# Optimization experiments

Hardware: AMD Instinct MI355X
Metric: run time of the kernel (lower is better)

Reference implementation:

```python
import jax, jax.numpy as jnp
import numpy as np

B, C, H, W = 2, 32, 128, 128
K = 5            # window_size
NH = 2           # num_heads
HD = C // NH     # head_dim = 16
KK = K * K
HID = int(2 * C * 2.0)  # mlp hidden = dim*2*mlp_ratio = 128
SCALE = HD ** -0.5


def _ln(x, w, b, eps=1e-5):
    m = jnp.mean(x, -1, keepdims=True)
    v = jnp.var(x, -1, keepdims=True)
    return (x - m) * jax.lax.rsqrt(v + eps) * w + b


def _windows(t):
    # t: [B,H,W,C] -> [B,H,W,C,K*K]; zero-padded KxK neighborhood per pixel
    # (same layout as nn.Unfold: kernel position is the fastest-varying axis).
    p = (K - 1) // 2
    Hc, Wc = t.shape[1], t.shape[2]
    tp = jnp.pad(t, ((0, 0), (p, p), (p, p), (0, 0)))
    return jnp.stack([tp[:, i:i + Hc, j:j + Wc, :] for i in range(K) for j in range(K)], axis=-1)


def _rel_index():
    # Swin-style relative position index for a KxK window -> [KK,KK] ints
    c = jnp.stack(jnp.meshgrid(jnp.arange(K), jnp.arange(K), indexing='ij'), 0).reshape(2, -1)
    r = (c[:, :, None] - c[:, None, :]).transpose(1, 2, 0) + (K - 1)
    return r[..., 0] * (2 * K - 1) + r[..., 1]


def _ckbd_mask(h, w):
    # checkerboard attention mask: [L, KK, KK] additive (0 or -100)
    ck = jnp.zeros((h, w), jnp.float32)
    ck = ck.at[0::2, 1::2].set(1.0).at[1::2, 0::2].set(1.0)
    cw = _windows(ck[None, :, :, None])[0, :, :, 0, :].reshape(h * w, KK)  # [L,KK]
    m = cw[:, :, None] * cw[:, None, :]
    return jnp.where(m == 1.0, 0.0, -100.0)


def setup_inputs() -> dict:
    key = jax.random.key(0)
    ks = jax.random.split(key, 8)
    p = lambda k, s: (0.02 * jax.random.normal(k, s)).astype(jnp.float32)
    return dict(
        x=jax.random.normal(ks[0], (B, C, H, W), dtype=jnp.float32),
        qkv_w=p(ks[1], (3 * C, C)), qkv_b=jnp.zeros((3 * C,), jnp.float32),
        rel_table=p(ks[2], ((2 * K - 1) ** 2, NH)),
        norm1_w=jnp.ones((C,), jnp.float32), norm1_b=jnp.zeros((C,), jnp.float32),
        norm2_w=jnp.ones((2 * C,), jnp.float32), norm2_b=jnp.zeros((2 * C,), jnp.float32),
        proj_w=p(ks[3], (2 * C, 2 * C)), proj_b=jnp.zeros((2 * C,), jnp.float32),
        fusion_w=p(ks[4], (2 * C, C, K, K)), fusion_b=jnp.zeros((2 * C,), jnp.float32),
        mlp_w1=p(ks[5], (HID, 2 * C)), mlp_b1=jnp.zeros((HID,), jnp.float32),
        mlp_w2=p(ks[6], (2 * C, HID)), mlp_b2=jnp.zeros((2 * C,), jnp.float32),
    )


def reference(x, qkv_w, qkv_b, rel_table, norm1_w, norm1_b, norm2_w, norm2_b,
              proj_w, proj_b, fusion_w, fusion_b, mlp_w1, mlp_b1, mlp_w2, mlp_b2):
    Bs, Cs, Hs, Ws = x.shape
    L = Hs * Ws
    xt = x.reshape(Bs, Cs, L).transpose(0, 2, 1)          # [B,L,C]
    xn = _ln(xt, norm1_w, norm1_b)
    qkv = jnp.einsum('blc,oc->blo', xn, qkv_w) + qkv_b     # [B,L,3C]
    qkv = qkv.reshape(Bs, Hs, Ws, 3, Cs)
    q, k, v = qkv[..., 0, :], qkv[..., 1, :], qkv[..., 2, :]  # each [B,H,W,C]

    def heads(t):
        # windows -> [B,L,C,KK]; split C as (head_dim, num_heads) to match the
        # original reshape(B,L,head_dim,num_heads,KK).permute(0,1,3,4,2)
        w_ = _windows(t).reshape(Bs, L, HD, NH, KK)
        return w_.transpose(0, 1, 3, 4, 2)                 # [B,L,nh,KK,hd]

    qh, kh, vh = heads(q), heads(k), heads(v)
    attn = jnp.einsum('blhqd,blhkd->blhqk', qh * SCALE, kh)  # [B,L,nh,KK,KK]

    bias = rel_table[_rel_index().reshape(-1)].reshape(KK, KK, NH).transpose(2, 0, 1)
    attn = attn + bias[None, None]
    attn = attn + _ckbd_mask(Hs, Ws)[None, :, None]
    attn = jax.nn.softmax(attn, axis=-1)

    o = jnp.einsum('blhqk,blhkd->blhqd', attn, vh)           # [B,L,nh,KK,hd]
    # -> [B,L,K,K,nh,hd] -> [B,L,K,K,C] (head-major channel order, as in torch)
    o = o.reshape(Bs, L, NH, K, K, HD).transpose(0, 1, 3, 4, 2, 5).reshape(Bs, L, K, K, Cs)
    # fusion: Conv2d(C, 2C, kernel=K) on [BL,C,K,K] with no padding == full contraction
    y = jnp.einsum('blijc,ocij->blo', o, fusion_w) + fusion_b  # [B,L,2C]
    y = jnp.einsum('blc,oc->blo', y, proj_w) + proj_b
    h1 = _ln(y, norm2_w, norm2_b)
    mlp = jnp.einsum('blh,oh->blo',
                     jax.nn.gelu(jnp.einsum('blc,hc->blh', h1, mlp_w1) + mlp_b1, approximate=False),
                     mlp_w2) + mlp_b2
    y = y + mlp
    return y.transpose(0, 2, 1).reshape(Bs, 2 * Cs, Hs, Ws)
```

## Files before the change

kernel.cpp:

```cpp
#include <hip/hip_runtime.h>
#include <cstdint>
#include <cstddef>

#define HH 128
#define WW 128
#define LL 16384
#define BL 32768

typedef float  f32x4  __attribute__((ext_vector_type(4)));
typedef __fp16 h2     __attribute__((ext_vector_type(2)));
typedef __fp16 h8     __attribute__((ext_vector_type(8)));

union U32H { unsigned u; h2 h; };

static __device__ __forceinline__ float fdot2(h2 a, h2 b, float c) {
  return __builtin_amdgcn_fdot2(a, b, c, false);
}
static __device__ __forceinline__ unsigned pkh2(float a, float b) {
  h2 h = __builtin_amdgcn_cvt_pkrtz(a, b);
  U32H t; t.h = h; return t.u;
}
static __device__ __forceinline__ h2 bcasth(float a) {
  return __builtin_amdgcn_cvt_pkrtz(a, a);
}
static __device__ __forceinline__ unsigned short f2h(float x) {
  union { __fp16 h; unsigned short u; } c; c.h = (__fp16)x; return c.u;
}

#define LOADH8(dst, ptr) { \
  uint4 _a = *(const uint4*)(ptr); uint4 _b = *(const uint4*)((ptr)+8); U32H _t; \
  _t.u=_a.x; dst[0]=_t.h; _t.u=_a.y; dst[1]=_t.h; _t.u=_a.z; dst[2]=_t.h; _t.u=_a.w; dst[3]=_t.h; \
  _t.u=_b.x; dst[4]=_t.h; _t.u=_b.y; dst[5]=_t.h; _t.u=_b.z; dst[6]=_t.h; _t.u=_b.w; dst[7]=_t.h; }

__global__ __launch_bounds__(256) void k_combine(
    const float* __restrict__ proj_w, const float* __restrict__ proj_b,
    const float* __restrict__ fw, const float* __restrict__ fb,
    const float* __restrict__ w1, const float* __restrict__ w2,
    unsigned short* __restrict__ wctT, float* __restrict__ bc,
    unsigned short* __restrict__ w1h, unsigned short* __restrict__ w2h)
{
  if (blockIdx.x == 200) {
    int o = threadIdx.x;
    if (o < 64) {
      float acc = proj_b[o];
      for (int m = 0; m < 64; ++m) acc = fmaf(proj_w[o*64+m], fb[m], acc);
      bc[o] = acc;
    }
    return;
  }
  if (blockIdx.x == 201) {
    for (int i = threadIdx.x; i < 8192; i += 256) w1h[i] = f2h(w1[i]);
    return;
  }
  if (blockIdx.x == 202) {
    for (int i = threadIdx.x; i < 8192; i += 256) w2h[i] = f2h(w2[i]);
    return;
  }
  int gid = blockIdx.x * 256 + threadIdx.x;
  int o  = gid / 800;
  int kk = gid - o * 800;
  int c  = kk & 31;
  int t  = kk >> 5;
  int in = c * 25 + t;
  float acc = 0.f;
  for (int m = 0; m < 64; ++m) acc = fmaf(proj_w[o*64+m], fw[m*800+in], acc);
  wctT[gid] = f2h(acc);
}

__global__ __launch_bounds__(128) void k_ln_qkv(
    const float* __restrict__ x, const float* __restrict__ qkv_w,
    const float* __restrict__ qkv_b, const float* __restrict__ n1w,
    const float* __restrict__ n1b, unsigned short* __restrict__ qo,
    unsigned short* __restrict__ ko, unsigned short* __restrict__ vo)
{
  __shared__ float sW[32*32];
  __shared__ float sB[32];
  __shared__ float sNw[32], sNb[32];
  int p = blockIdx.y;
  for (int i = threadIdx.x; i < 32*32; i += 128) sW[i] = qkv_w[p*1024 + i];
  if (threadIdx.x < 32) {
    sB[threadIdx.x]  = qkv_b[p*32 + threadIdx.x];
    sNw[threadIdx.x] = n1w[threadIdx.x];
    sNb[threadIdx.x] = n1b[threadIdx.x];
  }
  __syncthreads();
  int gid = blockIdx.x * 128 + threadIdx.x;
  int b = gid >> 14, l = gid & (LL - 1);
  const float* xp = x + (size_t)b * 32 * LL + l;
  float xv[32];
  float mean = 0.f;
  #pragma unroll
  for (int c = 0; c < 32; ++c) { xv[c] = xp[(size_t)c * LL]; mean += xv[c]; }
  mean *= 0.03125f;
  float var = 0.f;
  #pragma unroll
  for (int c = 0; c < 32; ++c) { float d = xv[c] - mean; var = fmaf(d, d, var); }
  float rs = rsqrtf(var * 0.03125f + 1e-5f);
  #pragma unroll
  for (int c = 0; c < 32; ++c) xv[c] = (xv[c] - mean) * rs * sNw[c] + sNb[c];
  float ao[32];
  #pragma unroll
  for (int o = 0; o < 32; ++o) {
    const float* wr = &sW[o * 32];
    float acc = sB[o];
    #pragma unroll
    for (int c = 0; c < 32; ++c) acc = fmaf(xv[c], wr[c], acc);
    ao[(o & 1) * 16 + (o >> 1)] = acc;
  }
  unsigned short* op = (p == 0 ? qo : p == 1 ? ko : vo) + (size_t)gid * 32;
  #pragma unroll
  for (int e = 0; e < 4; ++e) {
    uint4 pk4;
    pk4.x = pkh2(ao[e*8+0], ao[e*8+1]);
    pk4.y = pkh2(ao[e*8+2], ao[e*8+3]);
    pk4.z = pkh2(ao[e*8+4], ao[e*8+5]);
    pk4.w = pkh2(ao[e*8+6], ao[e*8+7]);
    *(uint4*)(op + e*8) = pk4;
  }
}

#define TH 4
#define TW 8
#define NPOS 96
#define KVSTR 24
#define OSTRU 524

template<int MODE>
static __device__ __forceinline__ void attn_pair(
    int tqA, int tqB, int nh, bool wA, bool wB,
    int posb, int sOrow, int klbase,
    const unsigned short* __restrict__ sQ, const unsigned short* __restrict__ sK,
    const unsigned short* __restrict__ sV, unsigned short* __restrict__ sO,
    const float* __restrict__ sRT, const float* __restrict__ sPar)
{
  const int nhb = nh * 96;
  int iqA = tqA / 5, jqA = tqA - iqA * 5;
  int iqB = tqB / 5, jqB = tqB - iqB * 5;
  int pqA = posb + iqA * 12 + jqA;
  int pqB = posb + iqB * 12 + jqB;
  float parqA = 0.f, parqB = 0.f;
  if (MODE == 3) { parqA = sPar[pqA]; parqB = sPar[pqB]; }
  h2 qA[8], qB[8];
  LOADH8(qA, &sQ[(nhb + pqA) * KVSTR]);
  LOADH8(qB, &sQ[(nhb + pqB) * KVSTR]);
  const int bbA = (iqA * 9 + jqA) * 2 + 80 + nh;
  const int bbB = (iqB * 9 + jqB) * 2 + 80 + nh;
  float sA = 0.f, sB = 0.f;
  h2 ooA[8], ooB[8];
  #pragma unroll
  for (int e = 0; e < 8; ++e) { ooA[e] = (h2)(__fp16)0.f; ooB[e] = (h2)(__fp16)0.f; }
  #pragma unroll 1
  for (int ik = 0; ik < 5; ++ik) {
    int pkrow = posb + ik * 12;
    int bA = bbA - ik * 18, bB = bbB - ik * 18;
    auto body = [&](int jk) {
      int pk = pkrow + jk;
      h2 kh[8];
      LOADH8(kh, &sK[(nhb + pk) * KVSTR]);
      float aA = 0.f, aB = 0.f;
      #pragma unroll
      for (int u = 0; u < 8; ++u) { aA = fdot2(qA[u], kh[u], aA); aB = fdot2(qB[u], kh[u], aB); }
      float biasA = sRT[bA - 2 * jk], biasB = sRT[bB - 2 * jk];
      float eA, eB;
      if (MODE == 3) {
        float park = sPar[pk];
        float mk = (park == 1.f) ? 0.f : -100.f;
        eA = __expf(fmaf(parqA, mk, fmaf(aA, 0.25f, biasA)));
        eB = __expf(fmaf(parqB, mk, fmaf(aB, 0.25f, biasB)));
      } else {
        eA = __expf(fmaf(aA, 0.25f, biasA));
        eB = __expf(fmaf(aB, 0.25f, biasB));
      }
      sA += eA; sB += eB;
      h2 eAh = bcasth(eA), eBh = bcasth(eB);
      h2 vh[8];
      LOADH8(vh, &sV[(nhb + pk) * KVSTR]);
      #pragma unroll
      for (int u = 0; u < 8; ++u) { ooA[u] = eAh * vh[u] + ooA[u]; ooB[u] = eBh * vh[u] + ooB[u]; }
    };
    if (MODE == 0 || MODE == 3) {
      body(0); body(1); body(2); body(3); body(4);
    } else if (MODE == 1) {
      if ((ik & 1) == 0) { body(1); body(3); }
      else { body(0); body(2); body(4); }
    } else {
      if ((ik & 1) == 0) { body(0); body(2); body(4); }
      else { body(1); body(3); }
    }
  }
  if (wA) {
    h2 ih = bcasth(1.f / sA);
    int kl = (tqA - klbase) * 32 + nh * 16;
    union { h2 h[8]; uint4 u4[2]; } R;
    #pragma unroll
    for (int u = 0; u < 8; ++u) R.h[u] = ooA[u] * ih;
    *(uint4*)&sO[sOrow * OSTRU + kl] = R.u4[0];
    *(uint4*)&sO[sOrow * OSTRU + kl + 8] = R.u4[1];
  }
  if (wB) {
    h2 ih = bcasth(1.f / sB);
    int kl = (tqB - klbase) * 32 + nh * 16;
    union { h2 h[8]; uint4 u4[2]; } R;
    #pragma unroll
    for (int u = 0; u < 8; ++u) R.h[u] = ooB[u] * ih;
    *(uint4*)&sO[sOrow * OSTRU + kl] = R.u4[0];
    *(uint4*)&sO[sOrow * OSTRU + kl + 8] = R.u4[1];
  }
}

__global__ __launch_bounds__(256, 3) void k_attn(
    const unsigned short* __restrict__ qi, const unsigned short* __restrict__ ki,
    const unsigned short* __restrict__ vi, const float* __restrict__ rel_table,
    const unsigned short* __restrict__ wctT, const float* __restrict__ bc,
    float* __restrict__ y2)
{
  __shared__ __align__(16) unsigned short sQ[192*KVSTR];
  __shared__ __align__(16) unsigned short sK[192*KVSTR];
  __shared__ __align__(16) unsigned short sV[192*KVSTR];
  __shared__ __align__(16) unsigned short sO[32*OSTRU];
  __shared__ float sRT[162];
  __shared__ float sPar[NPOS];

  int tid = threadIdx.x;
  int lane = tid & 63, wv = tid >> 6;
  int b  = blockIdx.z;
  int h0 = blockIdx.y * TH, w0 = blockIdx.x * TW;
  bool fastb = (blockIdx.y >= 1) && (blockIdx.y <= 30) && (blockIdx.x >= 1) && (blockIdx.x <= 14);

  for (int i = tid; i < 162; i += 256) sRT[i] = rel_table[i];
  if (tid < NPOS) {
    int ph = tid / 12, pw = tid - ph * 12;
    int h2v = h0 + ph - 2, w2v = w0 + pw - 2;
    bool valid = ((unsigned)h2v < HH) && ((unsigned)w2v < WW);
    sPar[tid] = (valid && (((h2v + w2v) & 1) == 1)) ? 1.f : 0.f;
  }
  for (int idx = tid; idx < 1152; idx += 256) {
    int arr = idx / 384;
    int rem = idx - arr * 384;
    int pos = rem >> 2, q4 = rem & 3;
    int nh = q4 >> 1, half = q4 & 1;
    int ph = pos / 12, pw = pos - ph * 12;
    int h2v = h0 + ph - 2, w2v = w0 + pw - 2;
    uint4 val = make_uint4(0u, 0u, 0u, 0u);
    if (((unsigned)h2v < HH) && ((unsigned)w2v < WW)) {
      const unsigned short* src = (arr == 0 ? ki : arr == 1 ? vi : qi)
                       + ((size_t)((b << 14) + (h2v << 7) + w2v)) * 32 + nh * 16 + half * 8;
      val = *(const uint4*)src;
    }
    unsigned short* dp = (arr == 0 ? sK : arr == 1 ? sV : sQ)
                       + (nh * 96 + pos) * KVSTR + half * 8;
    *(uint4*)dp = val;
  }
  __syncthreads();

  f32x4 acc[2] = {{0.f,0.f,0.f,0.f},{0.f,0.f,0.f,0.f}};
  int ocol = wv * 16 + (lane & 15);

  int cls = wv & 1;
  int l16 = lane & 15;
  int nh  = wv >> 1;
  int kk4 = lane >> 4;
  int ly  = l16 >> 2;
  int lx  = 2 * (l16 & 3) + ((cls + ly) & 1);
  int posb  = ly * 12 + lx;
  int sOrow = cls * 16 + l16;

  if (fastb) {
    if (cls == 0) {
      attn_pair<0>(4*kk4,   4*kk4+2, nh, true, true, posb, sOrow, 0, sQ, sK, sV, sO, sRT, sPar);
      attn_pair<1>(4*kk4+1, 4*kk4+3, nh, true, true, posb, sOrow, 0, sQ, sK, sV, sO, sRT, sPar);
    } else {
      attn_pair<0>(4*kk4+1, 4*kk4+3, nh, true, true, posb, sOrow, 0, sQ, sK, sV, sO, sRT, sPar);
      attn_pair<2>(4*kk4,   4*kk4+2, nh, true, true, posb, sOrow, 0, sQ, sK, sV, sO, sRT, sPar);
    }
  } else {
    attn_pair<3>(4*kk4,   4*kk4+2, nh, true, true, posb, sOrow, 0, sQ, sK, sV, sO, sRT, sPar);
    attn_pair<3>(4*kk4+1, 4*kk4+3, nh, true, true, posb, sOrow, 0, sQ, sK, sV, sO, sRT, sPar);
  }
  __syncthreads();
  {
    const unsigned short* bcol = wctT + (size_t)ocol * 800 + (lane >> 4) * 8;
    for (int kt = 0; kt < 16; ++kt) {
      h8 bfrag = *(const h8*)(bcol + kt * 32);
      #pragma unroll
      for (int mt = 0; mt < 2; ++mt) {
        h8 afrag = *(const h8*)&sO[(mt*16 + (lane & 15))*OSTRU + kt*32 + (lane >> 4)*8];
        acc[mt] = __builtin_amdgcn_mfma_f32_16x16x32_f16(afrag, bfrag, acc[mt], 0, 0, 0);
      }
    }
  }
  __syncthreads();

  {
    int LqA = 16, LqB = 18; bool LwA = false, LwB = false;
    int SqA = 17, SqB = 19; bool SwA = false, SwB = false;
    if (cls == 0) {
      if (kk4 == 0)      { LwA = LwB = true; SwA = SwB = true; }
      else if (kk4 == 1) { LqA = 20; LqB = 22; LwA = LwB = true; SqA = 21; SqB = 23; SwA = SwB = true; }
      else if (kk4 == 2) { LqA = 24; LqB = 24; LwA = true; }
    } else {
      if (kk4 == 0)      { LqA = 17; LqB = 19; LwA = LwB = true; SqA = 16; SqB = 18; SwA = SwB = true; }
      else if (kk4 == 1) { LqA = 21; LqB = 23; LwA = LwB = true; SqA = 20; SqB = 22; SwA = SwB = true; }
      else if (kk4 == 2) { SqA = 24; SqB = 24; SwA = true; }
    }
    if (fastb) {
      if (cls == 0) {
        attn_pair<0>(LqA, LqB, nh, LwA, LwB, posb, sOrow, 16, sQ, sK, sV, sO, sRT, sPar);
        attn_pair<1>(SqA, SqB, nh, SwA, SwB, posb, sOrow, 16, sQ, sK, sV, sO, sRT, sPar);
      } else {
        attn_pair<0>(LqA, LqB, nh, LwA, LwB, posb, sOrow, 16, sQ, sK, sV, sO, sRT, sPar);
        attn_pair<2>(SqA, SqB, nh, SwA, SwB, posb, sOrow, 16, sQ, sK, sV, sO, sRT, sPar);
      }
    } else {
      attn_pair<3>(LqA, LqB, nh, LwA, LwB, posb, sOrow, 16, sQ, sK, sV, sO, sRT, sPar);
      attn_pair<3>(SqA, SqB, nh, SwA, SwB, posb, sOrow, 16, sQ, sK, sV, sO, sRT, sPar);
    }
  }
  __syncthreads();
  {
    const unsigned short* bcol = wctT + (size_t)ocol * 800 + 512 + (lane >> 4) * 8;
    for (int kt = 0; kt < 9; ++kt) {
      h8 bfrag = *(const h8*)(bcol + kt * 32);
      #pragma unroll
      for (int mt = 0; mt < 2; ++mt) {
        h8 afrag = *(const h8*)&sO[(mt*16 + (lane & 15))*OSTRU + kt*32 + (lane >> 4)*8];
        acc[mt] = __builtin_amdgcn_mfma_f32_16x16x32_f16(afrag, bfrag, acc[mt], 0, 0, 0);
      }
    }
  }
  __syncthreads();

  float bco = bc[ocol];
  #pragma unroll
  for (int mt = 0; mt < 2; ++mt) {
    #pragma unroll
    for (int r2 = 0; r2 < 4; ++r2) {
      int ly2 = lane >> 4;
      int lx2 = 2 * r2 + ((mt + ly2) & 1);
      int gid = (b << 14) + ((h0 + ly2) << 7) + (w0 + lx2);
      y2[(size_t)gid * 64 + ocol] = acc[mt][r2] + bco;
    }
  }
}

__global__ __launch_bounds__(256) void k_mlp(
    const float* __restrict__ y2, const float* __restrict__ n2w,
    const float* __restrict__ n2b, const unsigned short* __restrict__ w1h,
    const float* __restrict__ b1, const unsigned short* __restrict__ w2h,
    const float* __restrict__ b2, float* __restrict__ out)
{
  __shared__ __align__(16) unsigned short sA[64*72];
  __shared__ __align__(16) unsigned short sH[64*136];
  int tid = threadIdx.x;
  int lane = tid & 63, wv = tid >> 6;
  int m0 = blockIdx.x * 64;
  {
    int r = tid >> 2, qd = tid & 3;
    const float* yp = y2 + (size_t)(m0 + r) * 64 + qd * 16;
    float xv[16];
    float s = 0.f;
    #pragma unroll
    for (int e = 0; e < 4; ++e) {
      float4 t4 = *(const float4*)(yp + e*4);
      xv[4*e] = t4.x; xv[4*e+1] = t4.y; xv[4*e+2] = t4.z; xv[4*e+3] = t4.w;
      s += t4.x + t4.y + t4.z + t4.w;
    }
    s += __shfl_xor(s, 1);
    s += __shfl_xor(s, 2);
    float mean = s * (1.f/64.f);
    float v = 0.f;
    #pragma unroll
    for (int e = 0; e < 16; ++e) { float d = xv[e] - mean; v = fmaf(d, d, v); }
    v += __shfl_xor(v, 1);
    v += __shfl_xor(v, 2);
    float rs = rsqrtf(v * (1.f/64.f) + 1e-5f);
    #pragma unroll
    for (int u = 0; u < 8; ++u) {
      int c0 = qd*16 + 2*u;
      float h0v = (xv[2*u]   - mean) * rs * n2w[c0]   + n2b[c0];
      float h1v = (xv[2*u+1] - mean) * rs * n2w[c0+1] + n2b[c0+1];
      *(unsigned*)&sA[r*72 + c0] = pkh2(h0v, h1v);
    }
  }
  __syncthreads();
  f32x4 acc1[4][2];
  #pragma unroll
  for (int mt = 0; mt < 4; ++mt)
    #pragma unroll
    for (int nt = 0; nt < 2; ++nt) acc1[mt][nt] = (f32x4){0.f,0.f,0.f,0.f};
  #pragma unroll
  for (int kt = 0; kt < 2; ++kt) {
    #pragma unroll
    for (int nt = 0; nt < 2; ++nt) {
      int ncol = wv*32 + nt*16 + (lane & 15);
      h8 bfrag = *(const h8*)(w1h + ncol*64 + kt*32 + (lane >> 4)*8);
      #pragma unroll
      for (int mt = 0; mt < 4; ++mt) {
        h8 afrag = *(const h8*)&sA[(mt*16 + (lane & 15))*72 + kt*32 + (lane >> 4)*8];
        acc1[mt][nt] = __builtin_amdgcn_mfma_f32_16x16x32_f16(afrag, bfrag, acc1[mt][nt], 0, 0, 0);
      }
    }
  }
  #pragma unroll
  for (int nt = 0; nt < 2; ++nt) {
    int ncol = wv*32 + nt*16 + (lane & 15);
    float b1v = b1[ncol];
    #pragma unroll
    for (int mt = 0; mt < 4; ++mt) {
      #pragma unroll
      for (int r2 = 0; r2 < 4; ++r2) {
        int mrow = mt*16 + (lane >> 4)*4 + r2;
        float h = acc1[mt][nt][r2] + b1v;
        float g = 0.5f * h * (1.f + erff(h * 0.70710678118f));
        sH[mrow*136 + ncol] = f2h(g);
      }
    }
  }
  __syncthreads();
  f32x4 acc2[4];
  #pragma unroll
  for (int mt = 0; mt < 4; ++mt) acc2[mt] = (f32x4){0.f,0.f,0.f,0.f};
  int ocol = wv*16 + (lane & 15);
  #pragma unroll
  for (int kt = 0; kt < 4; ++kt) {
    h8 bfrag = *(const h8*)(w2h + ocol*128 + kt*32 + (lane >> 4)*8);
    #pragma unroll
    for (int mt = 0; mt < 4; ++mt) {
      h8 afrag = *(const h8*)&sH[(mt*16 + (lane & 15))*136 + kt*32 + (lane >> 4)*8];
      acc2[mt] = __builtin_amdgcn_mfma_f32_16x16x32_f16(afrag, bfrag, acc2[mt], 0, 0, 0);
    }
  }
  float b2v = b2[ocol];
  int bb = m0 >> 14;
  #pragma unroll
  for (int mt = 0; mt < 4; ++mt) {
    int mrow = mt*16 + (lane >> 4)*4;
    int l = m0 + mrow;
    const float* yp = y2 + (size_t)l * 64 + ocol;
    float4 o4;
    o4.x = yp[0]   + acc2[mt][0] + b2v;
    o4.y = yp[64]  + acc2[mt][1] + b2v;
    o4.z = yp[128] + acc2[mt][2] + b2v;
    o4.w = yp[192] + acc2[mt][3] + b2v;
    *(float4*)&out[(size_t)bb * 64 * LL + (size_t)ocol * LL + (l - (bb << 14))] = o4;
  }
}

extern "C" void kernel_launch(void* const* d_in, const int* in_sizes, int n_in,
                              void* d_out, int out_size, void* d_ws, size_t ws_size,
                              hipStream_t stream) {
  const float* x         = (const float*)d_in[0];
  const float* qkv_w     = (const float*)d_in[1];
  const float* qkv_b     = (const float*)d_in[2];
  const float* rel_table = (const float*)d_in[3];
  const float* n1w       = (const float*)d_in[4];
  const float* n1b       = (const float*)d_in[5];
  const float* n2w       = (const float*)d_in[6];
  const float* n2b       = (const float*)d_in[7];
  const float* proj_w    = (const float*)d_in[8];
  const float* proj_b    = (const float*)d_in[9];
  const float* fw        = (const float*)d_in[10];
  const float* fb        = (const float*)d_in[11];
  const float* w1        = (const float*)d_in[12];
  const float* b1        = (const float*)d_in[13];
  const float* w2        = (const float*)d_in[14];
  const float* b2        = (const float*)d_in[15];

  char* ws = (char*)d_ws;
  unsigned short* q    = (unsigned short*)(ws);
  unsigned short* k    = (unsigned short*)(ws + 2097152);
  unsigned short* v    = (unsigned short*)(ws + 4194304);
  float*          y2   = (float*)(ws + 6291456);
  unsigned short* wctT = (unsigned short*)(ws + 14680064);
  float*          bc   = (float*)(ws + 14782464);
  unsigned short* w1h  = (unsigned short*)(ws + 14782720);
  unsigned short* w2h  = (unsigned short*)(ws + 14799104);
  float* out = (float*)d_out;

  k_combine<<<203, 256, 0, stream>>>(proj_w, proj_b, fw, fb, w1, w2, wctT, bc, w1h, w2h);
  k_ln_qkv<<<dim3(BL/128, 3), 128, 0, stream>>>(x, qkv_w, qkv_b, n1w, n1b, q, k, v);
  k_attn<<<dim3(WW/TW, HH/TH, 2), 256, 0, stream>>>(q, k, v, rel_table, wctT, bc, y2);
  k_mlp<<<BL/64, 256, 0, stream>>>(y2, n2w, n2b, w1h, b1, w2h, b2, out);
}
```

Before: 92.80 us.

## Halve attention tile height, read Q from global, restructure thread mapping

Shrinks the attention block tile from 4x8 to 2x8 pixels, which doubles the grid and cuts shared memory. Q is no longer staged in LDS and is read directly from global memory. The pair of queries per thread is reorganised into a long/short pair that shares K/V loads under the checkerboard parity, and launch bounds are raised to allow more resident blocks. The MLP kernel's row tile is also halved to 32 rows. Smaller tiles mean more halo reloads of K/V, and the uncoalesced per-thread global Q loads may cost latency.

```diff
diff --git a/kernel.cpp b/kernel.cpp
--- a/kernel.cpp
+++ b/kernel.cpp
@@ -119,105 +119,126 @@
   }
 }
 
-#define TH 4
+#define TH 2
 #define TW 8
-#define NPOS 96
+#define NPOS 72
 #define KVSTR 24
 #define OSTRU 524
 
-template<int MODE>
-static __device__ __forceinline__ void attn_pair(
-    int tqA, int tqB, int nh, bool wA, bool wB,
+template<int CLS, bool SLOW>
+static __device__ __forceinline__ void attn_ls(
+    int tqL, int tqS, bool wL, bool wS, int nh,
+    int h0, int w0, int ly, int lx, int b,
+    const unsigned short* __restrict__ qi,
     int posb, int sOrow, int klbase,
-    const unsigned short* __restrict__ sQ, const unsigned short* __restrict__ sK,
+    const unsigned short* __restrict__ sK,
     const unsigned short* __restrict__ sV, unsigned short* __restrict__ sO,
     const float* __restrict__ sRT, const float* __restrict__ sPar)
 {
-  const int nhb = nh * 96;
-  int iqA = tqA / 5, jqA = tqA - iqA * 5;
-  int iqB = tqB / 5, jqB = tqB - iqB * 5;
-  int pqA = posb + iqA * 12 + jqA;
-  int pqB = posb + iqB * 12 + jqB;
-  float parqA = 0.f, parqB = 0.f;
-  if (MODE == 3) { parqA = sPar[pqA]; parqB = sPar[pqB]; }
-  h2 qA[8], qB[8];
-  LOADH8(qA, &sQ[(nhb + pqA) * KVSTR]);
-  LOADH8(qB, &sQ[(nhb + pqB) * KVSTR]);
-  const int bbA = (iqA * 9 + jqA) * 2 + 80 + nh;
-  const int bbB = (iqB * 9 + jqB) * 2 + 80 + nh;
-  float sA = 0.f, sB = 0.f;
-  h2 ooA[8], ooB[8];
-  #pragma unroll
-  for (int e = 0; e < 8; ++e) { ooA[e] = (h2)(__fp16)0.f; ooB[e] = (h2)(__fp16)0.f; }
+  const int nhb = nh * 72;
+  int iqL = tqL / 5, jqL = tqL - iqL * 5;
+  int iqS = tqS / 5, jqS = tqS - iqS * 5;
+  int hqL = h0 + ly + iqL - 2, wqL = w0 + lx + jqL - 2;
+  int hqS = h0 + ly + iqS - 2, wqS = w0 + lx + jqS - 2;
+  h2 qL[8], qS[8];
+  float parqL = 0.f, parqS = 0.f;
+  if (SLOW) {
+    bool vL = ((unsigned)hqL < HH) && ((unsigned)wqL < WW);
+    bool vS = ((unsigned)hqS < HH) && ((unsigned)wqS < WW);
+    parqL = (vL && (((hqL + wqL) & 1) == 1)) ? 1.f : 0.f;
+    parqS = (vS && (((hqS + wqS) & 1) == 1)) ? 1.f : 0.f;
+    if (vL) {
+      LOADH8(qL, qi + ((size_t)((b<<14)+(hqL<<7)+wqL))*32 + nh*16);
+    } else {
+      for (int u = 0; u < 8; ++u) qL[u] = (h2)(__fp16)0.f;
+    }
+    if (vS) {
+      LOADH8(qS, qi + ((size_t)((b<<14)+(hqS<<7)+wqS))*32 + nh*16);
+    } else {
+      for (int u = 0; u < 8; ++u) qS[u] = (h2)(__fp16)0.f;
+    }
+  } else {
+    LOADH8(qL, qi + ((size_t)((b<<14)+(hqL<<7)+wqL))*32 + nh*16);
+    LOADH8(qS, qi + ((size_t)((b<<14)+(hqS<<7)+wqS))*32 + nh*16);
+  }
+  const int bbL = (iqL * 9 + jqL) * 2 + 80 + nh;
+  const int bbS = (iqS * 9 + jqS) * 2 + 80 + nh;
+  float sumL = 0.f, sumS = 0.f;
+  h2 ooL[8], ooS[8];
+  #pragma unroll
+  for (int e = 0; e < 8; ++e) { ooL[e] = (h2)(__fp16)0.f; ooS[e] = (h2)(__fp16)0.f; }
   #pragma unroll 1
   for (int ik = 0; ik < 5; ++ik) {
     int pkrow = posb + ik * 12;
-    int bA = bbA - ik * 18, bB = bbB - ik * 18;
-    auto body = [&](int jk) {
+    int bL = bbL - ik * 18, bS = bbS - ik * 18;
+    auto body = [&](int jk, bool doS) {
       int pk = pkrow + jk;
-      h2 kh[8];
-      LOADH8(kh, &sK[(nhb + pk) * KVSTR]);
-      float aA = 0.f, aB = 0.f;
-      #pragma unroll
-      for (int u = 0; u < 8; ++u) { aA = fdot2(qA[u], kh[u], aA); aB = fdot2(qB[u], kh[u], aB); }
-      float biasA = sRT[bA - 2 * jk], biasB = sRT[bB - 2 * jk];
-      float eA, eB;
-      if (MODE == 3) {
-        float park = sPar[pk];
-        float mk = (park == 1.f) ? 0.f : -100.f;
-        eA = __expf(fmaf(parqA, mk, fmaf(aA, 0.25f, biasA)));
-        eB = __expf(fmaf(parqB, mk, fmaf(aB, 0.25f, biasB)));
-      } else {
-        eA = __expf(fmaf(aA, 0.25f, biasA));
-        eB = __expf(fmaf(aB, 0.25f, biasB));
+      h2 kh[8]; LOADH8(kh, &sK[(nhb + pk) * KVSTR]);
+      h2 vh[8]; LOADH8(vh, &sV[(nhb + pk) * KVSTR]);
+      float mk = 0.f;
+      if (SLOW) { float park = sPar[pk]; mk = (park == 1.f) ? 0.f : -100.f; }
+      {
+        float a = 0.f;
+        #pragma unroll
+        for (int u = 0; u < 8; ++u) a = fdot2(qL[u], kh[u], a);
+        float e = SLOW ? __expf(fmaf(parqL, mk, fmaf(a, 0.25f, sRT[bL - 2*jk])))
+                       : __expf(fmaf(a, 0.25f, sRT[bL - 2*jk]));
+        sumL += e;
+        h2 eh = bcasth(e);
+        #pragma unroll
+        for (int u = 0; u < 8; ++u) ooL[u] = eh * vh[u] + ooL[u];
       }
-      sA += eA; sB += eB;
-      h2 eAh = bcasth(eA), eBh = bcasth(eB);
-      h2 vh[8];
-      LOADH8(vh, &sV[(nhb + pk) * KVSTR]);
-      #pragma unroll
-      for (int u = 0; u < 8; ++u) { ooA[u] = eAh * vh[u] + ooA[u]; ooB[u] = eBh * vh[u] + ooB[u]; }
+      if (doS) {
+        float a = 0.f;
+        #pragma unroll
+        for (int u = 0; u < 8; ++u) a = fdot2(qS[u], kh[u], a);
+        float e = SLOW ? __expf(fmaf(parqS, mk, fmaf(a, 0.25f, sRT[bS - 2*jk])))
+                       : __expf(fmaf(a, 0.25f, sRT[bS - 2*jk]));
+        sumS += e;
+        h2 eh = bcasth(e);
+        #pragma unroll
+        for (int u = 0; u < 8; ++u) ooS[u] = eh * vh[u] + ooS[u];
+      }
     };
-    if (MODE == 0 || MODE == 3) {
-      body(0); body(1); body(2); body(3); body(4);
-    } else if (MODE == 1) {
-      if ((ik & 1) == 0) { body(1); body(3); }
-      else { body(0); body(2); body(4); }
+    if (SLOW) {
+      body(0,true); body(1,true); body(2,true); body(3,true); body(4,true);
+    } else if (CLS == 0) {
+      if ((ik & 1) == 0) { body(0,false); body(1,true);  body(2,false); body(3,true);  body(4,false); }
+      else               { body(0,true);  body(1,false); body(2,true);  body(3,false); body(4,true); }
     } else {
-      if ((ik & 1) == 0) { body(0); body(2); body(4); }
-      else { body(1); body(3); }
-    }
-  }
-  if (wA) {
-    h2 ih = bcasth(1.f / sA);
-    int kl = (tqA - klbase) * 32 + nh * 16;
+      if ((ik & 1) == 0) { body(0,true);  body(1,false); body(2,true);  body(3,false); body(4,true); }
+      else               { body(0,false); body(1,true);  body(2,false); body(3,true);  body(4,false); }
+    }
+  }
+  if (wL) {
+    h2 ih = bcasth(1.f / sumL);
+    int kl = (tqL - klbase) * 32 + nh * 16;
     union { h2 h[8]; uint4 u4[2]; } R;
     #pragma unroll
-    for (int u = 0; u < 8; ++u) R.h[u] = ooA[u] * ih;
+    for (int u = 0; u < 8; ++u) R.h[u] = ooL[u] * ih;
     *(uint4*)&sO[sOrow * OSTRU + kl] = R.u4[0];
     *(uint4*)&sO[sOrow * OSTRU + kl + 8] = R.u4[1];
   }
-  if (wB) {
-    h2 ih = bcasth(1.f / sB);
-    int kl = (tqB - klbase) * 32 + nh * 16;
+  if (wS) {
+    h2 ih = bcasth(1.f / sumS);
+    int kl = (tqS - klbase) * 32 + nh * 16;
     union { h2 h[8]; uint4 u4[2]; } R;
     #pragma unroll
-    for (int u = 0; u < 8; ++u) R.h[u] = ooB[u] * ih;
+    for (int u = 0; u < 8; ++u) R.h[u] = ooS[u] * ih;
     *(uint4*)&sO[sOrow * OSTRU + kl] = R.u4[0];
     *(uint4*)&sO[sOrow * OSTRU + kl + 8] = R.u4[1];
   }
 }
 
-__global__ __launch_bounds__(256, 3) void k_attn(
+__global__ __launch_bounds__(256, 5) void k_attn(
     const unsigned short* __restrict__ qi, const unsigned short* __restrict__ ki,
     const unsigned short* __restrict__ vi, const float* __restrict__ rel_table,
     const unsigned short* __restrict__ wctT, const float* __restrict__ bc,
     float* __restrict__ y2)
 {
-  __shared__ __align__(16) unsigned short sQ[192*KVSTR];
-  __shared__ __align__(16) unsigned short sK[192*KVSTR];
-  __shared__ __align__(16) unsigned short sV[192*KVSTR];
-  __shared__ __align__(16) unsigned short sO[32*OSTRU];
+  __shared__ __align__(16) unsigned short sK[144*KVSTR];
+  __shared__ __align__(16) unsigned short sV[144*KVSTR];
+  __shared__ __align__(16) unsigned short sO[16*OSTRU];
   __shared__ float sRT[162];
   __shared__ float sPar[NPOS];
 
@@ -225,7 +246,7 @@
   int lane = tid & 63, wv = tid >> 6;
   int b  = blockIdx.z;
   int h0 = blockIdx.y * TH, w0 = blockIdx.x * TW;
-  bool fastb = (blockIdx.y >= 1) && (blockIdx.y <= 30) && (blockIdx.x >= 1) && (blockIdx.x <= 14);
+  bool fastb = (blockIdx.y >= 1) && (blockIdx.y <= 62) && (blockIdx.x >= 1) && (blockIdx.x <= 14);
 
   for (int i = tid; i < 162; i += 256) sRT[i] = rel_table[i];
   if (tid < NPOS) {
@@ -234,86 +255,69 @@
     bool valid = ((unsigned)h2v < HH) && ((unsigned)w2v < WW);
     sPar[tid] = (valid && (((h2v + w2v) & 1) == 1)) ? 1.f : 0.f;
   }
-  for (int idx = tid; idx < 1152; idx += 256) {
-    int arr = idx / 384;
-    int rem = idx - arr * 384;
+  for (int idx = tid; idx < 576; idx += 256) {
+    int arr = idx / 288;
+    int rem = idx - arr * 288;
     int pos = rem >> 2, q4 = rem & 3;
     int nh = q4 >> 1, half = q4 & 1;
     int ph = pos / 12, pw = pos - ph * 12;
     int h2v = h0 + ph - 2, w2v = w0 + pw - 2;
     uint4 val = make_uint4(0u, 0u, 0u, 0u);
     if (((unsigned)h2v < HH) && ((unsigned)w2v < WW)) {
-      const unsigned short* src = (arr == 0 ? ki : arr == 1 ? vi : qi)
+      const unsigned short* src = (arr == 0 ? ki : vi)
                        + ((size_t)((b << 14) + (h2v << 7) + w2v)) * 32 + nh * 16 + half * 8;
       val = *(const uint4*)src;
     }
-    unsigned short* dp = (arr == 0 ? sK : arr == 1 ? sV : sQ)
-                       + (nh * 96 + pos) * KVSTR + half * 8;
+    unsigned short* dp = (arr == 0 ? sK : sV) + (nh * 72 + pos) * KVSTR + half * 8;
     *(uint4*)dp = val;
   }
   __syncthreads();
 
-  f32x4 acc[2] = {{0.f,0.f,0.f,0.f},{0.f,0.f,0.f,0.f}};
+  f32x4 acc = {0.f, 0.f, 0.f, 0.f};
   int ocol = wv * 16 + (lane & 15);
 
   int cls = wv & 1;
-  int l16 = lane & 15;
   int nh  = wv >> 1;
-  int kk4 = lane >> 4;
-  int ly  = l16 >> 2;
-  int lx  = 2 * (l16 & 3) + ((cls + ly) & 1);
+  int l8  = lane & 7;
+  int r8  = lane >> 3;
+  int ly  = l8 >> 2;
+  int lx  = 2 * (l8 & 3) + ((cls + ly) & 1);
   int posb  = ly * 12 + lx;
-  int sOrow = cls * 16 + l16;
+  int sOrow = cls * 8 + l8;
 
   if (fastb) {
-    if (cls == 0) {
-      attn_pair<0>(4*kk4,   4*kk4+2, nh, true, true, posb, sOrow, 0, sQ, sK, sV, sO, sRT, sPar);
-      attn_pair<1>(4*kk4+1, 4*kk4+3, nh, true, true, posb, sOrow, 0, sQ, sK, sV, sO, sRT, sPar);
-    } else {
-      attn_pair<0>(4*kk4+1, 4*kk4+3, nh, true, true, posb, sOrow, 0, sQ, sK, sV, sO, sRT, sPar);
-      attn_pair<2>(4*kk4,   4*kk4+2, nh, true, true, posb, sOrow, 0, sQ, sK, sV, sO, sRT, sPar);
-    }
+    if (cls == 0) attn_ls<0,false>(2*r8,   2*r8+1, true, true, nh, h0,w0,ly,lx,b,qi, posb, sOrow, 0, sK, sV, sO, sRT, sPar);
+    else          attn_ls<1,false>(2*r8+1, 2*r8,   true, true, nh, h0,w0,ly,lx,b,qi, posb, sOrow, 0, sK, sV, sO, sRT, sPar);
   } else {
-    attn_pair<3>(4*kk4,   4*kk4+2, nh, true, true, posb, sOrow, 0, sQ, sK, sV, sO, sRT, sPar);
-    attn_pair<3>(4*kk4+1, 4*kk4+3, nh, true, true, posb, sOrow, 0, sQ, sK, sV, sO, sRT, sPar);
+    int tl = (cls == 0) ? 2*r8 : 2*r8+1;
+    int ts = (cls == 0) ? 2*r8+1 : 2*r8;
+    attn_ls<0,true>(tl, ts, true, true, nh, h0,w0,ly,lx,b,qi, posb, sOrow, 0, sK, sV, sO, sRT, sPar);
   }
   __syncthreads();
   {
     const unsigned short* bcol = wctT + (size_t)ocol * 800 + (lane >> 4) * 8;
     for (int kt = 0; kt < 16; ++kt) {
       h8 bfrag = *(const h8*)(bcol + kt * 32);
-      #pragma unroll
-      for (int mt = 0; mt < 2; ++mt) {
-        h8 afrag = *(const h8*)&sO[(mt*16 + (lane & 15))*OSTRU + kt*32 + (lane >> 4)*8];
-        acc[mt] = __builtin_amdgcn_mfma_f32_16x16x32_f16(afrag, bfrag, acc[mt], 0, 0, 0);
-      }
+      h8 afrag = *(const h8*)&sO[(lane & 15)*OSTRU + kt*32 + (lane >> 4)*8];
+      acc = __builtin_amdgcn_mfma_f32_16x16x32_f16(afrag, bfrag, acc, 0, 0, 0);
     }
   }
   __syncthreads();
 
   {
-    int LqA = 16, LqB = 18; bool LwA = false, LwB = false;
-    int SqA = 17, SqB = 19; bool SwA = false, SwB = false;
+    int tqL, tqS; bool wL, wS;
     if (cls == 0) {
-      if (kk4 == 0)      { LwA = LwB = true; SwA = SwB = true; }
-      else if (kk4 == 1) { LqA = 20; LqB = 22; LwA = LwB = true; SqA = 21; SqB = 23; SwA = SwB = true; }
-      else if (kk4 == 2) { LqA = 24; LqB = 24; LwA = true; }
+      tqL = (r8 < 5) ? 16 + 2*r8 : 16; wL = (r8 < 5);
+      tqS = (r8 < 4) ? 17 + 2*r8 : 17; wS = (r8 < 4);
     } else {
-      if (kk4 == 0)      { LqA = 17; LqB = 19; LwA = LwB = true; SqA = 16; SqB = 18; SwA = SwB = true; }
-      else if (kk4 == 1) { LqA = 21; LqB = 23; LwA = LwB = true; SqA = 20; SqB = 22; SwA = SwB = true; }
-      else if (kk4 == 2) { SqA = 24; SqB = 24; SwA = true; }
+      tqL = (r8 < 4) ? 17 + 2*r8 : 17; wL = (r8 < 4);
+      tqS = (r8 < 5) ? 16 + 2*r8 : 16; wS = (r8 < 5);
     }
     if (fastb) {
-      if (cls == 0) {
-        attn_pair<0>(LqA, LqB, nh, LwA, LwB, posb, sOrow, 16, sQ, sK, sV, sO, sRT, sPar);
-        attn_pair<1>(SqA, SqB, nh, SwA, SwB, posb, sOrow, 16, sQ, sK, sV, sO, sRT, sPar);
-      } else {
-        attn_pair<0>(LqA, LqB, nh, LwA, LwB, posb, sOrow, 16, sQ, sK, sV, sO, sRT, sPar);
-        attn_pair<2>(SqA, SqB, nh, SwA, SwB, posb, sOrow, 16, sQ, sK, sV, sO, sRT, sPar);
-      }
+      if (cls == 0) attn_ls<0,false>(tqL, tqS, wL, wS, nh, h0,w0,ly,lx,b,qi, posb, sOrow, 16, sK, sV, sO, sRT, sPar);
+      else          attn_ls<1,false>(tqL, tqS, wL, wS, nh, h0,w0,ly,lx,b,qi, posb, sOrow, 16, sK, sV, sO, sRT, sPar);
     } else {
-      attn_pair<3>(LqA, LqB, nh, LwA, LwB, posb, sOrow, 16, sQ, sK, sV, sO, sRT, sPar);
-      attn_pair<3>(SqA, SqB, nh, SwA, SwB, posb, sOrow, 16, sQ, sK, sV, sO, sRT, sPar);
+      attn_ls<0,true>(tqL, tqS, wL, wS, nh, h0,w0,ly,lx,b,qi, posb, sOrow, 16, sK, sV, sO, sRT, sPar);
     }
   }
   __syncthreads();
@@ -321,25 +325,20 @@
     const unsigned short* bcol = wctT + (size_t)ocol * 800 + 512 + (lane >> 4) * 8;
     for (int kt = 0; kt < 9; ++kt) {
       h8 bfrag = *(const h8*)(bcol + kt * 32);
-      #pragma unroll
-      for (int mt = 0; mt < 2; ++mt) {
-        h8 afrag = *(const h8*)&sO[(mt*16 + (lane & 15))*OSTRU + kt*32 + (lane >> 4)*8];
-        acc[mt] = __builtin_amdgcn_mfma_f32_16x16x32_f16(afrag, bfrag, acc[mt], 0, 0, 0);
-      }
+      h8 afrag = *(const h8*)&sO[(lane & 15)*OSTRU + kt*32 + (lane >> 4)*8];
+      acc = __builtin_amdgcn_mfma_f32_16x16x32_f16(afrag, bfrag, acc, 0, 0, 0);
     }
   }
   __syncthreads();
 
   float bco = bc[ocol];
   #pragma unroll
-  for (int mt = 0; mt < 2; ++mt) {
-    #pragma unroll
-    for (int r2 = 0; r2 < 4; ++r2) {
-      int ly2 = lane >> 4;
-      int lx2 = 2 * r2 + ((mt + ly2) & 1);
-      int gid = (b << 14) + ((h0 + ly2) << 7) + (w0 + lx2);
-      y2[(size_t)gid * 64 + ocol] = acc[mt][r2] + bco;
-    }
+  for (int r2 = 0; r2 < 4; ++r2) {
+    int r = (lane >> 4) * 4 + r2;
+    int cls2 = r >> 3, i8 = r & 7;
+    int ly2 = i8 >> 2, lx2 = 2 * (i8 & 3) + ((cls2 + ly2) & 1);
+    int gid = (b << 14) + ((h0 + ly2) << 7) + (w0 + lx2);
+    y2[(size_t)gid * 64 + ocol] = acc[r2] + bco;
   }
 }
 
@@ -349,43 +348,45 @@
     const float* __restrict__ b1, const unsigned short* __restrict__ w2h,
     const float* __restrict__ b2, float* __restrict__ out)
 {
-  __shared__ __align__(16) unsigned short sA[64*72];
-  __shared__ __align__(16) unsigned short sH[64*136];
+  __shared__ __align__(16) unsigned short sA[32*72];
+  __shared__ __align__(16) unsigned short sH[32*136];
   int tid = threadIdx.x;
   int lane = tid & 63, wv = tid >> 6;
-  int m0 = blockIdx.x * 64;
+  int m0 = blockIdx.x * 32;
   {
-    int r = tid >> 2, qd = tid & 3;
-    const float* yp = y2 + (size_t)(m0 + r) * 64 + qd * 16;
-    float xv[16];
+    int r = tid >> 3, qd = tid & 7;
+    const float* yp = y2 + (size_t)(m0 + r) * 64 + qd * 8;
+    float xv[8];
     float s = 0.f;
     #pragma unroll
-    for (int e = 0; e < 4; ++e) {
+    for (int e = 0; e < 2; ++e) {
       float4 t4 = *(const float4*)(yp + e*4);
       xv[4*e] = t4.x; xv[4*e+1] = t4.y; xv[4*e+2] = t4.z; xv[4*e+3] = t4.w;
       s += t4.x + t4.y + t4.z + t4.w;
     }
     s += __shfl_xor(s, 1);
     s += __shfl_xor(s, 2);
+    s += __shfl_xor(s, 4);
     float mean = s * (1.f/64.f);
     float v = 0.f;
     #pragma unroll
-    for (int e = 0; e < 16; ++e) { float d = xv[e] - mean; v = fmaf(d, d, v); }
+    for (int e = 0; e < 8; ++e) { float d = xv[e] - mean; v = fmaf(d, d, v); }
     v += __shfl_xor(v, 1);
     v += __shfl_xor(v, 2);
+    v += __shfl_xor(v, 4);
     float rs = rsqrtf(v * (1.f/64.f) + 1e-5f);
     #pragma unroll
-    for (int u = 0; u < 8; ++u) {
-      int c0 = qd*16 + 2*u;
+    for (int u = 0; u < 4; ++u) {
+      int c0 = qd*8 + 2*u;
       float h0v = (xv[2*u]   - mean) * rs * n2w[c0]   + n2b[c0];
       float h1v = (xv[2*u+1] - mean) * rs * n2w[c0+1] + n2b[c0+1];
       *(unsigned*)&sA[r*72 + c0] = pkh2(h0v, h1v);
     }
   }
   __syncthreads();
-  f32x4 acc1[4][2];
-  #pragma unroll
-  for (int mt = 0; mt < 4; ++mt)
+  f32x4 acc1[2][2];
+  #pragma unroll
+  for (int mt = 0; mt < 2; ++mt)
     #pragma unroll
     for (int nt = 0; nt < 2; ++nt) acc1[mt][nt] = (f32x4){0.f,0.f,0.f,0.f};
   #pragma unroll
@@ -395,7 +396,7 @@
       int ncol = wv*32 + nt*16 + (lane & 15);
       h8 bfrag = *(const h8*)(w1h + ncol*64 + kt*32 + (lane >> 4)*8);
       #pragma unroll
-      for (int mt = 0; mt < 4; ++mt) {
+      for (int mt = 0; mt < 2; ++mt) {
         h8 afrag = *(const h8*)&sA[(mt*16 + (lane & 15))*72 + kt*32 + (lane >> 4)*8];
         acc1[mt][nt] = __builtin_amdgcn_mfma_f32_16x16x32_f16(afrag, bfrag, acc1[mt][nt], 0, 0, 0);
       }
@@ -406,7 +407,7 @@
     int ncol = wv*32 + nt*16 + (lane & 15);
     float b1v = b1[ncol];
     #pragma unroll
-    for (int mt = 0; mt < 4; ++mt) {
+    for (int mt = 0; mt < 2; ++mt) {
       #pragma unroll
       for (int r2 = 0; r2 < 4; ++r2) {
         int mrow = mt*16 + (lane >> 4)*4 + r2;
@@ -417,15 +418,15 @@
     }
   }
   __syncthreads();
-  f32x4 acc2[4];
-  #pragma unroll
-  for (int mt = 0; mt < 4; ++mt) acc2[mt] = (f32x4){0.f,0.f,0.f,0.f};
+  f32x4 acc2[2];
+  #pragma unroll
+  for (int mt = 0; mt < 2; ++mt) acc2[mt] = (f32x4){0.f,0.f,0.f,0.f};
   int ocol = wv*16 + (lane & 15);
   #pragma unroll
   for (int kt = 0; kt < 4; ++kt) {
     h8 bfrag = *(const h8*)(w2h + ocol*128 + kt*32 + (lane >> 4)*8);
     #pragma unroll
-    for (int mt = 0; mt < 4; ++mt) {
+    for (int mt = 0; mt < 2; ++mt) {
       h8 afrag = *(const h8*)&sH[(mt*16 + (lane & 15))*136 + kt*32 + (lane >> 4)*8];
       acc2[mt] = __builtin_amdgcn_mfma_f32_16x16x32_f16(afrag, bfrag, acc2[mt], 0, 0, 0);
     }
@@ -433,7 +434,7 @@
   float b2v = b2[ocol];
   int bb = m0 >> 14;
   #pragma unroll
-  for (int mt = 0; mt < 4; ++mt) {
+  for (int mt = 0; mt < 2; ++mt) {
     int mrow = mt*16 + (lane >> 4)*4;
     int l = m0 + mrow;
     const float* yp = y2 + (size_t)l * 64 + ocol;
@@ -480,5 +481,5 @@
   k_combine<<<203, 256, 0, stream>>>(proj_w, proj_b, fw, fb, w1, w2, wctT, bc, w1h, w2h);
   k_ln_qkv<<<dim3(BL/128, 3), 128, 0, stream>>>(x, qkv_w, qkv_b, n1w, n1b, q, k, v);
   k_attn<<<dim3(WW/TW, HH/TH, 2), 256, 0, stream>>>(q, k, v, rel_table, wctT, bc, y2);
-  k_mlp<<<BL/64, 256, 0, stream>>>(y2, n2w, n2b, w1h, b1, w2h, b2, out);
-}
+  k_mlp<<<BL/32, 256, 0, stream>>>(y2, n2w, n2b, w1h, b1, w2h, b2, out);
+}
```

Result: faster. 88.05 us (-5.1%).
